# Kernel tuning notes

Hardware: AMD Instinct MI355X
Metric: run time of the kernel (lower is better)

## Reference

```python
import jax, jax.numpy as jnp
import numpy as np

N_NODES = 50000
N_EDGES = 640000
F_IN = 64
EDGE_DIM = 16
HID = 128
N_LAYERS = 3
N_CLASSES = 2
NUM_GRAPHS = 64
BN_EPS = 1e-5


def setup_inputs() -> dict:
    key = jax.random.key(0)
    ks = jax.random.split(key, 20)
    s = 0.05
    inp = {
        "x": jax.random.normal(ks[0], (N_NODES, F_IN), dtype=jnp.float32),
        "edge_index": jax.random.randint(ks[1], (2, N_EDGES), 0, N_NODES, dtype=jnp.int32),
        "edge_attr": jax.random.normal(ks[2], (N_EDGES, EDGE_DIM), dtype=jnp.float32),
        "batch": jnp.sort(jax.random.randint(ks[3], (N_NODES,), 0, NUM_GRAPHS, dtype=jnp.int32)),
        # node encoder
        "enc_W": jax.random.normal(ks[4], (F_IN, HID), dtype=jnp.float32) * s,
        "enc_b": jnp.zeros((HID,), dtype=jnp.float32),
        # per-layer GINEConv params (stacked over layers)
        "edge_W": jax.random.normal(ks[5], (N_LAYERS, EDGE_DIM, HID), dtype=jnp.float32) * s,
        "edge_b": jnp.zeros((N_LAYERS, HID), dtype=jnp.float32),
        "mlp_W1": jax.random.normal(ks[6], (N_LAYERS, HID, HID), dtype=jnp.float32) * s,
        "mlp_b1": jnp.zeros((N_LAYERS, HID), dtype=jnp.float32),
        "mlp_W2": jax.random.normal(ks[7], (N_LAYERS, HID, HID), dtype=jnp.float32) * s,
        "mlp_b2": jnp.zeros((N_LAYERS, HID), dtype=jnp.float32),
        "bn_gamma": jnp.ones((N_LAYERS, HID), dtype=jnp.float32),
        "bn_beta": jnp.zeros((N_LAYERS, HID), dtype=jnp.float32),
        # classification head
        "head_W1": jax.random.normal(ks[8], (HID, HID), dtype=jnp.float32) * s,
        "head_b1": jnp.zeros((HID,), dtype=jnp.float32),
        "head_W2": jax.random.normal(ks[9], (HID, N_CLASSES), dtype=jnp.float32) * s,
        "head_b2": jnp.zeros((N_CLASSES,), dtype=jnp.float32),
    }
    return inp


def reference(x, edge_index, edge_attr, batch, enc_W, enc_b, edge_W, edge_b,
              mlp_W1, mlp_b1, mlp_W2, mlp_b2, bn_gamma, bn_beta,
              head_W1, head_b1, head_W2, head_b2):
    src, dst = edge_index[0], edge_index[1]  # message flows src -> dst
    h = x @ enc_W + enc_b  # [N, HID]
    for l in range(N_LAYERS):
        # GINEConv: msg = ReLU(x_src + Lin(edge_attr)); aggr = scatter_add at dst
        e = edge_attr @ edge_W[l] + edge_b[l]          # [E, HID]
        msg = jax.nn.relu(h[src] + e)                  # [E, HID]
        agg = jax.ops.segment_sum(msg, dst, num_segments=N_NODES)
        z = h + agg  # (1 + eps) * x + aggr, eps = 0
        # node MLP: Linear-ReLU-Linear
        z = jax.nn.relu(z @ mlp_W1[l] + mlp_b1[l]) @ mlp_W2[l] + mlp_b2[l]
        # BatchNorm1d (training-mode batch stats) + ReLU (dropout = identity)
        mean = jnp.mean(z, axis=0)
        var = jnp.var(z, axis=0)
        z = bn_gamma[l] * (z - mean) * jax.lax.rsqrt(var + BN_EPS) + bn_beta[l]
        h = jax.nn.relu(z)
    # global_add_pool over graphs
    g = jax.ops.segment_sum(h, batch, num_segments=NUM_GRAPHS)  # [G, HID]
    out = jax.nn.relu(g @ head_W1 + head_b1) @ head_W2 + head_b2
    return out  # [G, N_CLASSES]
```

## Files before the change

### kernel.cpp

```cpp
#include <hip/hip_runtime.h>
#include <hip/hip_bf16.h>

#define N_NODES 50000
#define N_EDGES 640000
#define F_IN 64
#define EDGE_DIM 16
#define HID 128
#define N_LAYERS 3
#define NUM_GRAPHS 64
#define BN_EPS 1e-5f

typedef __attribute__((ext_vector_type(8))) short short8;
typedef __attribute__((ext_vector_type(4))) float f32x4;
typedef __attribute__((ext_vector_type(2))) __fp16 half2v;

__device__ __forceinline__ float bfl(unsigned int u) {
    unsigned int v = u << 16; float f; __builtin_memcpy(&f, &v, 4); return f;
}
__device__ __forceinline__ float bfh(unsigned int u) {
    unsigned int v = u & 0xffff0000u; float f; __builtin_memcpy(&f, &v, 4); return f;
}
__device__ __forceinline__ unsigned int f2bf(float f) {
    unsigned int v; __builtin_memcpy(&v, &f, 4);
    v += 0x7fffu + ((v >> 16) & 1u);
    return v >> 16;
}
__device__ __forceinline__ unsigned int pack2(float lo, float hi) {
    return f2bf(lo) | (f2bf(hi) << 16);
}
__device__ __forceinline__ half2v u2h(unsigned int u) {
    half2v h; __builtin_memcpy(&h, &u, 4); return h;
}
__device__ __forceinline__ unsigned int pkh(float a, float b) {
    half2v h = __builtin_amdgcn_cvt_pkrtz(a, b);
    unsigned int u; __builtin_memcpy(&u, &h, 4); return u;
}

__global__ void k_hist(const int* __restrict__ dst, int* __restrict__ deg) {
    int e = blockIdx.x * 256 + threadIdx.x;
    atomicAdd(&deg[dst[e]], 1);
}

__global__ void k_blockred(const int* __restrict__ deg, int* __restrict__ bsums) {
    __shared__ int s[256];
    int i = blockIdx.x * 256 + threadIdx.x;
    int v = (i < N_NODES) ? deg[i] : 0;
    s[threadIdx.x] = v;
    __syncthreads();
    for (int off = 128; off > 0; off >>= 1) {
        if (threadIdx.x < off) s[threadIdx.x] += s[threadIdx.x + off];
        __syncthreads();
    }
    if (threadIdx.x == 0) bsums[blockIdx.x] = s[0];
}

__global__ void k_scan_bsums(int* __restrict__ bsums, int nb) {
    __shared__ int s[256];
    const int tid = threadIdx.x;
    const int v = (tid < nb) ? bsums[tid] : 0;
    s[tid] = v;
    __syncthreads();
    for (int off = 1; off < 256; off <<= 1) {
        int t = 0;
        if (tid >= off) t = s[tid - off];
        __syncthreads();
        s[tid] += t;
        __syncthreads();
    }
    if (tid < nb) bsums[tid] = s[tid] - v;
}

__global__ void k_scan_blocks(int* __restrict__ deg_rowptr, const int* __restrict__ bsums,
                              int* __restrict__ cursor) {
    __shared__ int s[256];
    int tid = threadIdx.x;
    int i = blockIdx.x * 256 + tid;
    int v = (i < N_NODES) ? deg_rowptr[i] : 0;
    s[tid] = v;
    __syncthreads();
    for (int off = 1; off < 256; off <<= 1) {
        int t = 0;
        if (tid >= off) t = s[tid - off];
        __syncthreads();
        s[tid] += t;
        __syncthreads();
    }
    int excl = s[tid] - v + bsums[blockIdx.x];
    if (i < N_NODES) {
        deg_rowptr[i] = excl;
        cursor[i] = excl;
    }
    if (i == N_NODES - 1) deg_rowptr[N_NODES] = N_EDGES;
}

__global__ void k_fill(const int* __restrict__ dst, int* __restrict__ cursor,
                       int* __restrict__ elist) {
    int e = blockIdx.x * 256 + threadIdx.x;
    int p = atomicAdd(&cursor[dst[e]], 1);
    elist[p] = e;
}

__global__ __launch_bounds__(256) void k_gather(const int* __restrict__ elist,
                                                const int* __restrict__ esrc,
                                                const float* __restrict__ eattr,
                                                int* __restrict__ src_s,
                                                uint4* __restrict__ eattr_h) {
    const int base = blockIdx.x * 1024;
    const int tid = threadIdx.x;
    int p[4], eid[4];
#pragma unroll
    for (int j = 0; j < 4; ++j) p[j] = base + tid + j * 256;
#pragma unroll
    for (int j = 0; j < 4; ++j) eid[j] = elist[p[j]];
    int sv[4];
#pragma unroll
    for (int j = 0; j < 4; ++j) sv[j] = esrc[eid[j]];
    float4 a[4][4];
#pragma unroll
    for (int j = 0; j < 4; ++j) {
        const float* ep = eattr + (size_t)eid[j] * EDGE_DIM;
        a[j][0] = *(const float4*)ep;
        a[j][1] = *(const float4*)(ep + 4);
        a[j][2] = *(const float4*)(ep + 8);
        a[j][3] = *(const float4*)(ep + 12);
    }
#pragma unroll
    for (int j = 0; j < 4; ++j) {
        src_s[p[j]] = sv[j];
        eattr_h[p[j] * 2] = make_uint4(pkh(a[j][0].x, a[j][0].y), pkh(a[j][0].z, a[j][0].w),
                                       pkh(a[j][1].x, a[j][1].y), pkh(a[j][1].z, a[j][1].w));
        eattr_h[p[j] * 2 + 1] = make_uint4(pkh(a[j][2].x, a[j][2].y), pkh(a[j][2].z, a[j][2].w),
                                           pkh(a[j][3].x, a[j][3].y), pkh(a[j][3].z, a[j][3].w));
    }
}

__global__ void k_pack(const float* __restrict__ W1, const float* __restrict__ W2,
                       const float* __restrict__ encW, const float* __restrict__ eW,
                       unsigned short* __restrict__ wp, unsigned short* __restrict__ wpe,
                       unsigned int* __restrict__ wek) {
    const int t = blockIdx.x * 256 + threadIdx.x;
    if (t < 12288) {
        const int mat = t >> 11;
        const int r = t & 2047;
        const int kstep = r >> 9;
        const int ntile = (r >> 6) & 7;
        const int lane = r & 63;
        const float* W = (mat < 3) ? (W1 + mat * 16384) : (W2 + (mat - 3) * 16384);
        const int kbase = kstep * 32 + ((lane >> 4) << 3);
        const int n = ntile * 16 + (lane & 15);
        unsigned int o[4];
#pragma unroll
        for (int jj = 0; jj < 4; ++jj)
            o[jj] = pack2(W[(kbase + 2 * jj) * HID + n], W[(kbase + 2 * jj + 1) * HID + n]);
        *(uint4*)(wp + (size_t)mat * 16384 + (((kstep << 3) + ntile) * 64 + lane) * 8) =
            make_uint4(o[0], o[1], o[2], o[3]);
    } else if (t < 13312) {
        const int r = t - 12288;
        const int kstep = r >> 9;
        const int ntile = (r >> 6) & 7;
        const int lane = r & 63;
        const int kbase = kstep * 32 + ((lane >> 4) << 3);
        const int n = ntile * 16 + (lane & 15);
        unsigned int o[4];
#pragma unroll
        for (int jj = 0; jj < 4; ++jj)
            o[jj] = pack2(encW[(kbase + 2 * jj) * HID + n], encW[(kbase + 2 * jj + 1) * HID + n]);
        *(uint4*)(wpe + (((kstep << 3) + ntile) * 64 + lane) * 8) =
            make_uint4(o[0], o[1], o[2], o[3]);
    } else {
        const int r = t - 13312;
        const int l = r >> 10;
        const int rr = r & 1023;
        const int kp = rr >> 7, f = rr & 127;
        const float a = eW[(l * EDGE_DIM + 2 * kp) * HID + f];
        const float b = eW[(l * EDGE_DIM + 2 * kp + 1) * HID + f];
        wek[r] = pkh(a, b);
    }
}

__global__ __launch_bounds__(256, 3) void k_encm(const float* __restrict__ x,
                                                 const unsigned short* __restrict__ wpe,
                                                 const float* __restrict__ b,
                                                 unsigned short* __restrict__ hb) {
    const int tid = threadIdx.x;
    const int w = tid >> 6, lane = tid & 63;
    const int q = lane >> 4, l15 = lane & 15;
    const int row0 = blockIdx.x * 64 + w * 16;
    const int ar = min(row0 + l15, N_NODES - 1);
    const float* xp = x + (size_t)ar * F_IN + q * 8;
    f32x4 acc[8];
#pragma unroll
    for (int nt = 0; nt < 8; ++nt) acc[nt] = (f32x4){0.f, 0.f, 0.f, 0.f};
#pragma unroll
    for (int ks = 0; ks < 2; ++ks) {
        const float4 v0 = *(const float4*)(xp + ks * 32);
        const float4 v1 = *(const float4*)(xp + ks * 32 + 4);
        unsigned int u[4] = {pack2(v0.x, v0.y), pack2(v0.z, v0.w),
                             pack2(v1.x, v1.y), pack2(v1.z, v1.w)};
        short8 a; __builtin_memcpy(&a, u, 16);
#pragma unroll
        for (int nt = 0; nt < 8; ++nt) {
            const short8 bf = *(const short8*)(wpe + (((ks << 3) + nt) * 64 + lane) * 8);
            acc[nt] = __builtin_amdgcn_mfma_f32_16x16x32_bf16(a, bf, acc[nt], 0, 0, 0);
        }
    }
    const int rowb = row0 + q * 4;
#pragma unroll
    for (int nt = 0; nt < 8; ++nt) {
        const float bias = b[nt * 16 + l15];
        const int cc = nt * 16 + l15;
#pragma unroll
        for (int reg = 0; reg < 4; ++reg) {
            const int r = rowb + reg;
            if (r < N_NODES)
                hb[(size_t)r * HID + cc] = (unsigned short)f2bf(acc[nt][reg] + bias);
        }
    }
}

__global__ __launch_bounds__(256, 2) void k_agg(const unsigned int* __restrict__ in32,
                                                const int* __restrict__ src_s,
                                                const uint4* __restrict__ eattr_h,
                                                const unsigned int* __restrict__ wek,
                                                const float* __restrict__ be,
                                                const int* __restrict__ row_ptr,
                                                const float* __restrict__ bnst,
                                                const float* __restrict__ gamma,
                                                const float* __restrict__ beta,
                                                const int bnmode,
                                                unsigned int* __restrict__ zb32) {
    const int lane = threadIdx.x & 63;
    const int wv = threadIdx.x >> 6;
    const int f2 = lane * 2;
    half2v wx[8], wy[8];
#pragma unroll
    for (int j = 0; j < 8; ++j) {
        wx[j] = u2h(wek[j * 128 + f2]);
        wy[j] = u2h(wek[j * 128 + f2 + 1]);
    }
    const float2 eb = *(const float2*)&be[f2];

    float2 sc = make_float2(1.f, 1.f), sh = make_float2(0.f, 0.f);
    float rlo = -3.4e38f;
    if (bnmode) {
        const float invN = 1.0f / (float)N_NODES;
        const float m0 = bnst[f2] * invN, m1 = bnst[f2 + 1] * invN;
        const float v0 = fmaxf(bnst[128 + f2] * invN - m0 * m0, 0.f);
        const float v1 = fmaxf(bnst[128 + f2 + 1] * invN - m1 * m1, 0.f);
        const float r0 = rsqrtf(v0 + BN_EPS), r1 = rsqrtf(v1 + BN_EPS);
        sc = make_float2(gamma[f2] * r0, gamma[f2 + 1] * r1);
        sh = make_float2(fmaf(-m0, sc.x, beta[f2]), fmaf(-m1, sc.y, beta[f2 + 1]));
        rlo = 0.f;
    }

    const int n = blockIdx.x * 4 + wv;
    const int base = __builtin_amdgcn_readfirstlane(row_ptr[n]);
    const int deg = __builtin_amdgcn_readfirstlane(row_ptr[n + 1]) - base;

    const unsigned int uself = in32[n * 64 + lane];
    float2 acc = make_float2(fmaxf(fmaf(bfl(uself), sc.x, sh.x), rlo),
                             fmaxf(fmaf(bfh(uself), sc.y, sh.y), rlo));

    if (deg > 0) {
        const int* sp = src_s + base;
        const uint4* ep = eattr_h + (size_t)base * 2;
        const int last = deg - 1;
        const int nch = (deg + 3) >> 2;

        unsigned int huC[4], huN[4];
        uint4 eaC[4][2], eaN[4][2];
        int s2[4];
        {
            int s0[4], s1[4];
#pragma unroll
            for (int j = 0; j < 4; ++j) s0[j] = sp[min(j, last)];
#pragma unroll
            for (int j = 0; j < 4; ++j) huC[j] = in32[s0[j] * 64 + lane];
#pragma unroll
            for (int j = 0; j < 4; ++j) s1[j] = sp[min(4 + j, last)];
            if (nch > 1) {
#pragma unroll
                for (int j = 0; j < 4; ++j) huN[j] = in32[s1[j] * 64 + lane];
            } else {
#pragma unroll
                for (int j = 0; j < 4; ++j) huN[j] = 0u;
            }
#pragma unroll
            for (int j = 0; j < 4; ++j) {
                const int e = min(j, last);
                eaC[j][0] = ep[e * 2]; eaC[j][1] = ep[e * 2 + 1];
            }
#pragma unroll
            for (int j = 0; j < 4; ++j) s2[j] = sp[min(8 + j, last)];
        }
        for (int c = 0; c < nch; ++c) {
            unsigned int huNN[4] = {0u, 0u, 0u, 0u};
            if (c + 2 < nch) {
#pragma unroll
                for (int j = 0; j < 4; ++j) huNN[j] = in32[s2[j] * 64 + lane];
            }
            int s3[4];
#pragma unroll
            for (int j = 0; j < 4; ++j) s3[j] = sp[min((c + 3) * 4 + j, last)];
            if (c + 1 < nch) {
#pragma unroll
                for (int j = 0; j < 4; ++j) {
                    const int e = min((c + 1) * 4 + j, last);
                    eaN[j][0] = ep[e * 2]; eaN[j][1] = ep[e * 2 + 1];
                }
            }
            __builtin_amdgcn_sched_barrier(0);
            const int rem = deg - c * 4;
#pragma unroll
            for (int j = 0; j < 4; ++j) {
                if (j < rem) {
                    const unsigned int* au = (const unsigned int*)&eaC[j][0];
                    float ex = eb.x, ey = eb.y;
#pragma unroll
                    for (int k = 0; k < 8; ++k) {
                        const half2v a = u2h(au[k]);
                        ex = __builtin_amdgcn_fdot2(a, wx[k], ex, false);
                        ey = __builtin_amdgcn_fdot2(a, wy[k], ey, false);
                    }
                    const float hx = fmaxf(fmaf(bfl(huC[j]), sc.x, sh.x), rlo);
                    const float hy = fmaxf(fmaf(bfh(huC[j]), sc.y, sh.y), rlo);
                    acc.x += fmaxf(hx + ex, 0.f);
                    acc.y += fmaxf(hy + ey, 0.f);
                }
            }
            if (c + 1 < nch) {
#pragma unroll
                for (int j = 0; j < 4; ++j) {
                    huC[j] = huN[j]; huN[j] = huNN[j];
                    eaC[j][0] = eaN[j][0]; eaC[j][1] = eaN[j][1];
                    s2[j] = s3[j];
                }
            }
        }
    }
    zb32[n * 64 + lane] = pack2(acc.x, acc.y);
}

#define Z1LD 136

__global__ __launch_bounds__(256, 3) void k_mlp(const unsigned short* __restrict__ zb,
                                                const unsigned short* __restrict__ w1p,
                                                const float* __restrict__ b1,
                                                const unsigned short* __restrict__ w2p,
                                                const float* __restrict__ b2,
                                                unsigned short* __restrict__ z2b,
                                                float* __restrict__ bn) {
    __shared__ unsigned short z1s[64 * Z1LD];
    __shared__ float redA[512];
    __shared__ float redB[512];
    const int tid = threadIdx.x;
    const int w = tid >> 6, lane = tid & 63;
    const int q = lane >> 4, l15 = lane & 15;
    const int row0 = blockIdx.x * 64 + w * 16;

    const int ar = min(row0 + l15, N_NODES - 1);
    const unsigned short* aptr = zb + (size_t)ar * HID + q * 8;

    f32x4 acc[8];
#pragma unroll
    for (int nt = 0; nt < 8; ++nt) acc[nt] = (f32x4){0.f, 0.f, 0.f, 0.f};

#pragma unroll
    for (int ks = 0; ks < 4; ++ks) {
        const short8 a = *(const short8*)(aptr + ks * 32);
#pragma unroll
        for (int nt = 0; nt < 8; ++nt) {
            const short8 b = *(const short8*)(w1p + (((ks << 3) + nt) * 64 + lane) * 8);
            acc[nt] = __builtin_amdgcn_mfma_f32_16x16x32_bf16(a, b, acc[nt], 0, 0, 0);
        }
    }
    {
        const int lr0 = w * 16 + q * 4;
#pragma unroll
        for (int nt = 0; nt < 8; ++nt) {
            const float bias = b1[nt * 16 + l15];
            const int cc = nt * 16 + l15;
#pragma unroll
            for (int reg = 0; reg < 4; ++reg) {
                const float v = fmaxf(acc[nt][reg] + bias, 0.f);
                z1s[(lr0 + reg) * Z1LD + cc] = (unsigned short)f2bf(v);
            }
        }
    }
#pragma unroll
    for (int nt = 0; nt < 8; ++nt) acc[nt] = (f32x4){0.f, 0.f, 0.f, 0.f};
    const unsigned short* a2p = &z1s[(w * 16 + l15) * Z1LD + q * 8];
#pragma unroll
    for (int ks = 0; ks < 4; ++ks) {
        const short8 a = *(const short8*)(a2p + ks * 32);
#pragma unroll
        for (int nt = 0; nt < 8; ++nt) {
            const short8 b = *(const short8*)(w2p + (((ks << 3) + nt) * 64 + lane) * 8);
            acc[nt] = __builtin_amdgcn_mfma_f32_16x16x32_bf16(a, b, acc[nt], 0, 0, 0);
        }
    }
    float s[8], sq[8];
    const int rowb = row0 + q * 4;
#pragma unroll
    for (int nt = 0; nt < 8; ++nt) {
        const float bias = b2[nt * 16 + l15];
        const int cc = nt * 16 + l15;
        float ls = 0.f, lq = 0.f;
#pragma unroll
        for (int reg = 0; reg < 4; ++reg) {
            const int r = rowb + reg;
            const float v = acc[nt][reg] + bias;
            if (r < N_NODES) {
                z2b[(size_t)r * HID + cc] = (unsigned short)f2bf(v);
                ls += v;
                lq = fmaf(v, v, lq);
            }
        }
        s[nt] = ls; sq[nt] = lq;
    }
#pragma unroll
    for (int nt = 0; nt < 8; ++nt) {
        s[nt] += __shfl_xor(s[nt], 16, 64);
        s[nt] += __shfl_xor(s[nt], 32, 64);
        sq[nt] += __shfl_xor(sq[nt], 16, 64);
        sq[nt] += __shfl_xor(sq[nt], 32, 64);
    }
    if (lane < 16) {
#pragma unroll
        for (int nt = 0; nt < 8; ++nt) {
            redA[w * 128 + nt * 16 + lane] = s[nt];
            redB[w * 128 + nt * 16 + lane] = sq[nt];
        }
    }
    __syncthreads();
    if (tid < 128) {
        float t = redA[tid] + redA[128 + tid] + redA[256 + tid] + redA[384 + tid];
        atomicAdd(&bn[tid], t);
    } else {
        const int c = tid - 128;
        float t = redB[c] + redB[128 + c] + redB[256 + c] + redB[384 + c];
        atomicAdd(&bn[128 + c], t);
    }
}

__global__ void k_pool(const unsigned short* __restrict__ z2b, const int* __restrict__ batch,
                       const float* __restrict__ bnst, const float* __restrict__ gamma,
                       const float* __restrict__ beta, float* __restrict__ g) {
    const int f = threadIdx.x;
    const float invN = 1.0f / (float)N_NODES;
    const float m = bnst[f] * invN;
    const float var = fmaxf(bnst[128 + f] * invN - m * m, 0.f);
    const float r = rsqrtf(var + BN_EPS);
    const float sc = gamma[f] * r;
    const float sh = fmaf(-m, sc, beta[f]);

    const int n0 = blockIdx.x * 128;
    const int nend = min(n0 + 128, N_NODES);
    float acc = 0.f;
    int cur = batch[n0];
    for (int n = n0; n < nend; ++n) {
        const int bb = batch[n];
        if (bb != cur) {
            atomicAdd(&g[cur * HID + f], acc);
            acc = 0.f;
            cur = bb;
        }
        const float raw = bfl((unsigned int)z2b[n * HID + f]);
        acc += fmaxf(fmaf(raw, sc, sh), 0.f);
    }
    atomicAdd(&g[cur * HID + f], acc);
}

__global__ void k_head1(const float* __restrict__ g, const float* __restrict__ W,
                        const float* __restrict__ b, float* __restrict__ g1) {
    const int idx = blockIdx.x * 256 + threadIdx.x;
    const int r = idx >> 7, c = idx & 127;
    float acc = b[c];
    for (int k = 0; k < 128; ++k) acc = fmaf(g[r * HID + k], W[k * HID + c], acc);
    g1[idx] = fmaxf(acc, 0.f);
}

__global__ void k_head2(const float* __restrict__ g1, const float* __restrict__ W,
                        const float* __restrict__ b, float* __restrict__ out) {
    const int idx = threadIdx.x;
    const int r = idx >> 1, c = idx & 1;
    float acc = b[c];
    for (int k = 0; k < 128; ++k) acc = fmaf(g1[r * HID + k], W[k * 2 + c], acc);
    out[idx] = acc;
}

extern "C" void kernel_launch(void* const* d_in, const int* in_sizes, int n_in,
                              void* d_out, int out_size, void* d_ws, size_t ws_size,
                              hipStream_t stream) {
    const float* x     = (const float*)d_in[0];
    const int*   ei    = (const int*)d_in[1];
    const float* eattr = (const float*)d_in[2];
    const int*   batch = (const int*)d_in[3];
    const float* encW  = (const float*)d_in[4];
    const float* encb  = (const float*)d_in[5];
    const float* eW    = (const float*)d_in[6];
    const float* eb    = (const float*)d_in[7];
    const float* W1    = (const float*)d_in[8];
    const float* b1    = (const float*)d_in[9];
    const float* W2    = (const float*)d_in[10];
    const float* b2    = (const float*)d_in[11];
    const float* gam   = (const float*)d_in[12];
    const float* bet   = (const float*)d_in[13];
    const float* hW1   = (const float*)d_in[14];
    const float* hb1   = (const float*)d_in[15];
    const float* hW2   = (const float*)d_in[16];
    const float* hb2   = (const float*)d_in[17];
    float* out = (float*)d_out;

    float* ws = (float*)d_ws;
    unsigned short* z2b = (unsigned short*)ws;
    float* bn  = ws + 3200000;
    float* g   = ws + 3200256;
    float* g1  = ws + 3208448;
    unsigned short* hb = (unsigned short*)(ws + 3216640);
    unsigned int* zb32 = (unsigned int*)(ws + 6416640);
    int* row_ptr = (int*)(ws + 11216640);
    int* cursor  = row_ptr + N_NODES + 1;
    int* elist   = cursor + N_NODES;
    int* bsums   = elist + N_EDGES;
    int* src_s   = bsums + 256;
    uint4* eattr_h = (uint4*)(ws + 12596900);
    unsigned short* wp  = (unsigned short*)(ws + 17716900);
    unsigned short* wpe = (unsigned short*)(ws + 17766100);
    unsigned int*   wek = (unsigned int*)(ws + 17770200);

    const int* esrc = ei;
    const int* edst = ei + N_EDGES;

    hipMemsetAsync(row_ptr, 0, (N_NODES + 1) * sizeof(int), stream);
    k_hist<<<N_EDGES / 256, 256, 0, stream>>>(edst, row_ptr);
    k_blockred<<<196, 256, 0, stream>>>(row_ptr, bsums);
    k_scan_bsums<<<1, 256, 0, stream>>>(bsums, 196);
    k_scan_blocks<<<196, 256, 0, stream>>>(row_ptr, bsums, cursor);
    k_fill<<<N_EDGES / 256, 256, 0, stream>>>(edst, cursor, elist);
    k_gather<<<N_EDGES / 1024, 256, 0, stream>>>(elist, esrc, eattr, src_s, eattr_h);

    k_pack<<<64, 256, 0, stream>>>(W1, W2, encW, eW, wp, wpe, wek);

    k_encm<<<782, 256, 0, stream>>>(x, wpe, encb, hb);

    for (int l = 0; l < N_LAYERS; ++l) {
        const unsigned int* in32 = (l == 0) ? (const unsigned int*)hb
                                            : (const unsigned int*)z2b;
        k_agg<<<12500, 256, 0, stream>>>(in32, src_s, eattr_h,
                                         wek + l * 1024, eb + l * HID, row_ptr,
                                         bn, gam + (l ? (l - 1) * HID : 0),
                                         bet + (l ? (l - 1) * HID : 0),
                                         (l > 0) ? 1 : 0, zb32);
        hipMemsetAsync(bn, 0, 256 * sizeof(float), stream);
        k_mlp<<<782, 256, 0, stream>>>((const unsigned short*)zb32,
                                       wp + (size_t)l * 16384, b1 + l * HID,
                                       wp + (size_t)(3 + l) * 16384, b2 + l * HID,
                                       z2b, bn);
    }

    hipMemsetAsync(g, 0, NUM_GRAPHS * HID * sizeof(float), stream);
    k_pool<<<391, 128, 0, stream>>>(z2b, batch, bn, gam + 2 * HID, bet + 2 * HID, g);
    k_head1<<<32, 256, 0, stream>>>(g, hW1, hb1, g1);
    k_head2<<<1, 128, 0, stream>>>(g1, hW2, hb2, out);
}
```

Measured before the change: 571.1 us.

## Cut kernel launches: fuse CSR build, memsets, and head layers

Replaces the three-kernel prefix scan with a single 1024-thread block scan. It merges the fill and gather steps so edges scatter their source and fp16 edge attributes straight to their CSR slot, which removes the elist indirection. Memsets are folded into the pack kernel and into k_agg, which now zeroes the BN accumulator through ping-pong buffers. The two head kernels are fused into one. The aim is to cut launch count and one pass over the edges, at the cost of a serial single-block scan.

```diff
diff --git a/kernel.cpp b/kernel.cpp
--- a/kernel.cpp
+++ b/kernel.cpp
@@ -41,103 +41,70 @@
     atomicAdd(&deg[dst[e]], 1);
 }
 
-__global__ void k_blockred(const int* __restrict__ deg, int* __restrict__ bsums) {
-    __shared__ int s[256];
-    int i = blockIdx.x * 256 + threadIdx.x;
-    int v = (i < N_NODES) ? deg[i] : 0;
-    s[threadIdx.x] = v;
+#define SCAN_CH 49
+__global__ __launch_bounds__(1024) void k_scan(int* __restrict__ rp,
+                                               int* __restrict__ cursor) {
+    __shared__ int s[1024];
+    const int tid = threadIdx.x;
+    const int base = tid * SCAN_CH;
+    int loc[SCAN_CH];
+    int sum = 0;
+#pragma unroll
+    for (int j = 0; j < SCAN_CH; ++j) {
+        const int i = base + j;
+        const int v = (i < N_NODES) ? rp[i] : 0;
+        loc[j] = sum;
+        sum += v;
+    }
+    s[tid] = sum;
     __syncthreads();
-    for (int off = 128; off > 0; off >>= 1) {
-        if (threadIdx.x < off) s[threadIdx.x] += s[threadIdx.x + off];
-        __syncthreads();
-    }
-    if (threadIdx.x == 0) bsums[blockIdx.x] = s[0];
-}
-
-__global__ void k_scan_bsums(int* __restrict__ bsums, int nb) {
-    __shared__ int s[256];
-    const int tid = threadIdx.x;
-    const int v = (tid < nb) ? bsums[tid] : 0;
-    s[tid] = v;
-    __syncthreads();
-    for (int off = 1; off < 256; off <<= 1) {
+    for (int off = 1; off < 1024; off <<= 1) {
         int t = 0;
         if (tid >= off) t = s[tid - off];
         __syncthreads();
         s[tid] += t;
         __syncthreads();
     }
-    if (tid < nb) bsums[tid] = s[tid] - v;
-}
-
-__global__ void k_scan_blocks(int* __restrict__ deg_rowptr, const int* __restrict__ bsums,
-                              int* __restrict__ cursor) {
-    __shared__ int s[256];
-    int tid = threadIdx.x;
-    int i = blockIdx.x * 256 + tid;
-    int v = (i < N_NODES) ? deg_rowptr[i] : 0;
-    s[tid] = v;
-    __syncthreads();
-    for (int off = 1; off < 256; off <<= 1) {
-        int t = 0;
-        if (tid >= off) t = s[tid - off];
-        __syncthreads();
-        s[tid] += t;
-        __syncthreads();
-    }
-    int excl = s[tid] - v + bsums[blockIdx.x];
-    if (i < N_NODES) {
-        deg_rowptr[i] = excl;
-        cursor[i] = excl;
-    }
-    if (i == N_NODES - 1) deg_rowptr[N_NODES] = N_EDGES;
-}
-
-__global__ void k_fill(const int* __restrict__ dst, int* __restrict__ cursor,
-                       int* __restrict__ elist) {
-    int e = blockIdx.x * 256 + threadIdx.x;
-    int p = atomicAdd(&cursor[dst[e]], 1);
-    elist[p] = e;
-}
-
-__global__ __launch_bounds__(256) void k_gather(const int* __restrict__ elist,
-                                                const int* __restrict__ esrc,
-                                                const float* __restrict__ eattr,
-                                                int* __restrict__ src_s,
-                                                uint4* __restrict__ eattr_h) {
-    const int base = blockIdx.x * 1024;
-    const int tid = threadIdx.x;
-    int p[4], eid[4];
-#pragma unroll
-    for (int j = 0; j < 4; ++j) p[j] = base + tid + j * 256;
-#pragma unroll
-    for (int j = 0; j < 4; ++j) eid[j] = elist[p[j]];
-    int sv[4];
-#pragma unroll
-    for (int j = 0; j < 4; ++j) sv[j] = esrc[eid[j]];
-    float4 a[4][4];
-#pragma unroll
-    for (int j = 0; j < 4; ++j) {
-        const float* ep = eattr + (size_t)eid[j] * EDGE_DIM;
-        a[j][0] = *(const float4*)ep;
-        a[j][1] = *(const float4*)(ep + 4);
-        a[j][2] = *(const float4*)(ep + 8);
-        a[j][3] = *(const float4*)(ep + 12);
-    }
-#pragma unroll
-    for (int j = 0; j < 4; ++j) {
-        src_s[p[j]] = sv[j];
-        eattr_h[p[j] * 2] = make_uint4(pkh(a[j][0].x, a[j][0].y), pkh(a[j][0].z, a[j][0].w),
-                                       pkh(a[j][1].x, a[j][1].y), pkh(a[j][1].z, a[j][1].w));
-        eattr_h[p[j] * 2 + 1] = make_uint4(pkh(a[j][2].x, a[j][2].y), pkh(a[j][2].z, a[j][2].w),
-                                           pkh(a[j][3].x, a[j][3].y), pkh(a[j][3].z, a[j][3].w));
-    }
+    const int offset = s[tid] - sum;
+#pragma unroll
+    for (int j = 0; j < SCAN_CH; ++j) {
+        const int i = base + j;
+        if (i < N_NODES) {
+            const int e = offset + loc[j];
+            rp[i] = e;
+            cursor[i] = e;
+        }
+    }
+    if (tid == 0) rp[N_NODES] = N_EDGES;
+}
+
+__global__ __launch_bounds__(256) void k_fillg(const int* __restrict__ esrc,
+                                               const int* __restrict__ edst,
+                                               const float* __restrict__ eattr,
+                                               int* __restrict__ cursor,
+                                               int* __restrict__ src_s,
+                                               uint4* __restrict__ eattr_h) {
+    const int e = blockIdx.x * 256 + threadIdx.x;
+    const int d = edst[e];
+    const int sv = esrc[e];
+    const float* ep = eattr + (size_t)e * EDGE_DIM;
+    const float4 a0 = *(const float4*)ep;
+    const float4 a1 = *(const float4*)(ep + 4);
+    const float4 a2 = *(const float4*)(ep + 8);
+    const float4 a3 = *(const float4*)(ep + 12);
+    const int p = atomicAdd(&cursor[d], 1);
+    src_s[p] = sv;
+    eattr_h[p * 2] = make_uint4(pkh(a0.x, a0.y), pkh(a0.z, a0.w),
+                                pkh(a1.x, a1.y), pkh(a1.z, a1.w));
+    eattr_h[p * 2 + 1] = make_uint4(pkh(a2.x, a2.y), pkh(a2.z, a2.w),
+                                    pkh(a3.x, a3.y), pkh(a3.z, a3.w));
 }
 
 __global__ void k_pack(const float* __restrict__ W1, const float* __restrict__ W2,
                        const float* __restrict__ encW, const float* __restrict__ eW,
                        unsigned short* __restrict__ wp, unsigned short* __restrict__ wpe,
-                       unsigned int* __restrict__ wek) {
+                       unsigned int* __restrict__ wek, float* __restrict__ g,
+                       int* __restrict__ row_ptr) {
     const int t = blockIdx.x * 256 + threadIdx.x;
     if (t < 12288) {
         const int mat = t >> 11;
@@ -167,7 +134,7 @@
             o[jj] = pack2(encW[(kbase + 2 * jj) * HID + n], encW[(kbase + 2 * jj + 1) * HID + n]);
         *(uint4*)(wpe + (((kstep << 3) + ntile) * 64 + lane) * 8) =
             make_uint4(o[0], o[1], o[2], o[3]);
-    } else {
+    } else if (t < 16384) {
         const int r = t - 13312;
         const int l = r >> 10;
         const int rr = r & 1023;
@@ -175,6 +142,10 @@
         const float a = eW[(l * EDGE_DIM + 2 * kp) * HID + f];
         const float b = eW[(l * EDGE_DIM + 2 * kp + 1) * HID + f];
         wek[r] = pkh(a, b);
+    } else if (t < 24576) {
+        g[t - 16384] = 0.f;
+    } else if (t < 24576 + N_NODES + 1) {
+        row_ptr[t - 24576] = 0;
     }
 }
 
@@ -228,7 +199,10 @@
                                                 const float* __restrict__ gamma,
                                                 const float* __restrict__ beta,
                                                 const int bnmode,
+                                                float* __restrict__ bnz,
                                                 unsigned int* __restrict__ zb32) {
+    if (blockIdx.x == 0) bnz[threadIdx.x] = 0.f;
+
     const int lane = threadIdx.x & 63;
     const int wv = threadIdx.x >> 6;
     const int f2 = lane * 2;
@@ -471,22 +445,29 @@
     atomicAdd(&g[cur * HID + f], acc);
 }
 
-__global__ void k_head1(const float* __restrict__ g, const float* __restrict__ W,
-                        const float* __restrict__ b, float* __restrict__ g1) {
-    const int idx = blockIdx.x * 256 + threadIdx.x;
-    const int r = idx >> 7, c = idx & 127;
-    float acc = b[c];
-    for (int k = 0; k < 128; ++k) acc = fmaf(g[r * HID + k], W[k * HID + c], acc);
-    g1[idx] = fmaxf(acc, 0.f);
-}
-
-__global__ void k_head2(const float* __restrict__ g1, const float* __restrict__ W,
-                        const float* __restrict__ b, float* __restrict__ out) {
-    const int idx = threadIdx.x;
-    const int r = idx >> 1, c = idx & 1;
-    float acc = b[c];
-    for (int k = 0; k < 128; ++k) acc = fmaf(g1[r * HID + k], W[k * 2 + c], acc);
-    out[idx] = acc;
+__global__ __launch_bounds__(1024) void k_head(const float* __restrict__ g,
+                                               const float* __restrict__ W1h,
+                                               const float* __restrict__ b1h,
+                                               const float* __restrict__ W2h,
+                                               const float* __restrict__ b2h,
+                                               float* __restrict__ out) {
+    __shared__ float g1s[NUM_GRAPHS * HID];
+    const int tid = threadIdx.x;
+#pragma unroll
+    for (int i = 0; i < 8; ++i) {
+        const int idx = i * 1024 + tid;
+        const int r = idx >> 7, c = idx & 127;
+        float acc = b1h[c];
+        for (int k = 0; k < 128; ++k) acc = fmaf(g[r * HID + k], W1h[k * HID + c], acc);
+        g1s[idx] = fmaxf(acc, 0.f);
+    }
+    __syncthreads();
+    if (tid < NUM_GRAPHS * 2) {
+        const int r = tid >> 1, c = tid & 1;
+        float acc = b2h[c];
+        for (int k = 0; k < 128; ++k) acc = fmaf(g1s[r * HID + k], W2h[k * 2 + c], acc);
+        out[tid] = acc;
+    }
 }
 
 extern "C" void kernel_launch(void* const* d_in, const int* in_sizes, int n_in,
@@ -514,16 +495,14 @@
 
     float* ws = (float*)d_ws;
     unsigned short* z2b = (unsigned short*)ws;
-    float* bn  = ws + 3200000;
-    float* g   = ws + 3200256;
-    float* g1  = ws + 3208448;
+    float* bn0 = ws + 3200000;
+    float* bn1 = ws + 3200256;
+    float* g   = ws + 3200512;
     unsigned short* hb = (unsigned short*)(ws + 3216640);
     unsigned int* zb32 = (unsigned int*)(ws + 6416640);
     int* row_ptr = (int*)(ws + 11216640);
     int* cursor  = row_ptr + N_NODES + 1;
-    int* elist   = cursor + N_NODES;
-    int* bsums   = elist + N_EDGES;
-    int* src_s   = bsums + 256;
+    int* src_s   = cursor + N_NODES;
     uint4* eattr_h = (uint4*)(ws + 12596900);
     unsigned short* wp  = (unsigned short*)(ws + 17716900);
     unsigned short* wpe = (unsigned short*)(ws + 17766100);
@@ -532,35 +511,30 @@
     const int* esrc = ei;
     const int* edst = ei + N_EDGES;
 
-    hipMemsetAsync(row_ptr, 0, (N_NODES + 1) * sizeof(int), stream);
+    k_pack<<<292, 256, 0, stream>>>(W1, W2, encW, eW, wp, wpe, wek, g, row_ptr);
     k_hist<<<N_EDGES / 256, 256, 0, stream>>>(edst, row_ptr);
-    k_blockred<<<196, 256, 0, stream>>>(row_ptr, bsums);
-    k_scan_bsums<<<1, 256, 0, stream>>>(bsums, 196);
-    k_scan_blocks<<<196, 256, 0, stream>>>(row_ptr, bsums, cursor);
-    k_fill<<<N_EDGES / 256, 256, 0, stream>>>(edst, cursor, elist);
-    k_gather<<<N_EDGES / 1024, 256, 0, stream>>>(elist, esrc, eattr, src_s, eattr_h);
-
-    k_pack<<<64, 256, 0, stream>>>(W1, W2, encW, eW, wp, wpe, wek);
+    k_scan<<<1, 1024, 0, stream>>>(row_ptr, cursor);
+    k_fillg<<<N_EDGES / 256, 256, 0, stream>>>(esrc, edst, eattr, cursor, src_s, eattr_h);
 
     k_encm<<<782, 256, 0, stream>>>(x, wpe, encb, hb);
 
+    float* bnbuf[2] = {bn0, bn1};
     for (int l = 0; l < N_LAYERS; ++l) {
         const unsigned int* in32 = (l == 0) ? (const unsigned int*)hb
                                             : (const unsigned int*)z2b;
+        float* bnRead = bnbuf[(l + 1) & 1];
+        float* bnZero = bnbuf[l & 1];
         k_agg<<<12500, 256, 0, stream>>>(in32, src_s, eattr_h,
                                          wek + l * 1024, eb + l * HID, row_ptr,
-                                         bn, gam + (l ? (l - 1) * HID : 0),
+                                         bnRead, gam + (l ? (l - 1) * HID : 0),
                                          bet + (l ? (l - 1) * HID : 0),
-                                         (l > 0) ? 1 : 0, zb32);
-        hipMemsetAsync(bn, 0, 256 * sizeof(float), stream);
+                                         (l > 0) ? 1 : 0, bnZero, zb32);
         k_mlp<<<782, 256, 0, stream>>>((const unsigned short*)zb32,
                                        wp + (size_t)l * 16384, b1 + l * HID,
                                        wp + (size_t)(3 + l) * 16384, b2 + l * HID,
-                                       z2b, bn);
-    }
-
-    hipMemsetAsync(g, 0, NUM_GRAPHS * HID * sizeof(float), stream);
-    k_pool<<<391, 128, 0, stream>>>(z2b, batch, bn, gam + 2 * HID, bet + 2 * HID, g);
-    k_head1<<<32, 256, 0, stream>>>(g, hW1, hb1, g1);
-    k_head2<<<1, 128, 0, stream>>>(g1, hW2, hb2, out);
-}
+                                       z2b, bnZero);
+    }
+
+    k_pool<<<391, 128, 0, stream>>>(z2b, batch, bn0, gam + 2 * HID, bet + 2 * HID, g);
+    k_head<<<1, 1024, 0, stream>>>(g, hW1, hb1, hW2, hb2, out);
+}
```

Result: slower. 674.0 us (+18.0%).
